# Performance work log

Hardware: AMD Instinct MI355X
Metric: run time of the kernel (lower is better)

The kernel has to match this reference:

```python
import jax, jax.numpy as jnp
import numpy as np

N_HEAD = 16


def setup_inputs() -> dict:
    key = jax.random.key(0)
    k1, k2, k3 = jax.random.split(key, 3)
    B, S, D = 2, 2048, 1024
    return {
        "hidden_states": jax.random.normal(k1, (B, S, D), dtype=jnp.float32),
        "c_attn_w": jax.random.normal(k2, (D, 3 * D), dtype=jnp.float32) * 0.02,
        "c_attn_b": jnp.zeros((3 * D,), dtype=jnp.float32),
        "c_proj_w": jax.random.normal(k3, (D, D), dtype=jnp.float32) * 0.02,
        "c_proj_b": jnp.zeros((D,), dtype=jnp.float32),
    }


def reference(hidden_states, c_attn_w, c_attn_b, c_proj_w, c_proj_b):
    B, S, D = hidden_states.shape
    H = N_HEAD
    hd = D // H
    # Fused QKV projection (Conv1D == linear with transposed weight layout)
    qkv = hidden_states @ c_attn_w + c_attn_b  # [B,S,3D]
    q, k, v = jnp.split(qkv, 3, axis=-1)
    # split heads -> [B,H,S,hd]
    q = q.reshape(B, S, H, hd).transpose(0, 2, 1, 3)
    k = k.reshape(B, S, H, hd).transpose(0, 2, 1, 3)
    v = v.reshape(B, S, H, hd).transpose(0, 2, 1, 3)
    # scaled dot-product with causal mask
    scores = jnp.einsum("bhqd,bhkd->bhqk", q, k) / jnp.asarray(hd ** 0.5, q.dtype)
    causal = jnp.tril(jnp.ones((S, S), dtype=bool))  # [S,S]
    mask_value = jnp.finfo(scores.dtype).min
    scores = jnp.where(causal[None, None, :, :], scores, mask_value)
    attn_weights = jax.nn.softmax(scores, axis=-1)  # [B,H,S,S]
    ctx = jnp.einsum("bhqk,bhkd->bhqd", attn_weights, v)  # [B,H,S,hd]
    ctx = ctx.transpose(0, 2, 1, 3).reshape(B, S, D)  # merge heads
    out = ctx @ c_proj_w + c_proj_b  # [B,S,D]
    return out
```

## Files before the change

### kernel.cpp

```cpp
#include <hip/hip_runtime.h>
#include <hip/hip_bf16.h>

typedef __attribute__((ext_vector_type(8))) short short8;
typedef __attribute__((ext_vector_type(4))) float f32x4;
typedef __attribute__((ext_vector_type(16))) float f32x16;
typedef __attribute__((ext_vector_type(4))) unsigned short u16x4;
typedef __attribute__((ext_vector_type(4))) unsigned int u32x4;

#define MFMA16(a, b, c) __builtin_amdgcn_mfma_f32_16x16x32_bf16((a), (b), (c), 0, 0, 0)
#define MFMA32(a, b, c) __builtin_amdgcn_mfma_f32_32x32x16_bf16((a), (b), (c), 0, 0, 0)

__device__ __forceinline__ unsigned short f2bf(float f) {
    union { float f; unsigned u; } v; v.f = f;
    return (unsigned short)((v.u + 0x7fffu + ((v.u >> 16) & 1u)) >> 16);
}

__device__ __forceinline__ unsigned cvtpk(float lo, float hi_) {
    unsigned r;
    asm volatile("v_cvt_pk_bf16_f32 %0, %1, %2" : "=v"(r) : "v"(lo), "v"(hi_));
    return r;
}

__global__ void cast_x_kernel(const float* __restrict__ x, ushort* __restrict__ y) {
    int i = blockIdx.x * blockDim.x + threadIdx.x;
    float4 v = ((const float4*)x)[i];
    u16x4 o = { f2bf(v.x), f2bf(v.y), f2bf(v.z), f2bf(v.w) };
    *(u16x4*)(y + (size_t)i * 4) = o;
}

__global__ void transpose_cast_kernel(const float* __restrict__ W, ushort* __restrict__ WT,
                                      int K, int N) {
    __shared__ ushort t[64][66];
    int n0 = blockIdx.x * 64, k0 = blockIdx.y * 64;
    int tn = threadIdx.x & 63, tg = threadIdx.x >> 6;
#pragma unroll
    for (int i = 0; i < 16; ++i) {
        int k = tg * 16 + i;
        t[tn][k] = f2bf(W[(size_t)(k0 + k) * N + n0 + tn]);
    }
    __syncthreads();
#pragma unroll
    for (int i = 0; i < 16; ++i) {
        int nn = tg * 16 + i;
        WT[(size_t)(n0 + nn) * K + k0 + tn] = t[nn][tn];
    }
}

#define QSCALE 0.18033688011112042f

template <int MODE>
__global__ __launch_bounds__(256)
void gemm_bt_kernel(const ushort* __restrict__ A, const ushort* __restrict__ BT,
                    const float* __restrict__ bias,
                    ushort* __restrict__ Qb, ushort* __restrict__ Kb,
                    ushort* __restrict__ VT, float* __restrict__ Out,
                    int M, int N, int K) {
    __shared__ ushort Asm[2][128 * 64];
    __shared__ ushort Bsm[2][128 * 64];
    const int lane = threadIdx.x & 63;
    const int wv = threadIdx.x >> 6;
    const int l15 = lane & 15, lg = lane >> 4;
    const int rm = (wv >> 1) * 64, cn = (wv & 1) * 64;
    const int row0 = blockIdx.y * 128, col0 = blockIdx.x * 128;

    const char* Agb = (const char*)(A + (size_t)row0 * K);
    const char* Bgb = (const char*)(BT + (size_t)col0 * K);
    const size_t rowbytes = (size_t)K * 2;

    f32x4 acc[4][4];
#pragma unroll
    for (int mi = 0; mi < 4; ++mi)
#pragma unroll
        for (int ni = 0; ni < 4; ++ni) acc[mi][ni] = f32x4{0.f, 0.f, 0.f, 0.f};

    const int grow_l = (lane >> 3);
    const int gcol_l = (lane & 7) * 16;

#define GSTAGE(buf, k0_)                                                                \
    do {                                                                                \
        _Pragma("unroll")                                                               \
        for (int c_ = 0; c_ < 4; ++c_) {                                                \
            int chunk = wv * 4 + c_;                              \
            size_t go = (size_t)(chunk * 8 + grow_l) * rowbytes + (size_t)(k0_)*2 +     \
                        gcol_l;                                                         \
            int lo = chunk * 1024 + lane * 16;                                          \
            __builtin_amdgcn_global_load_lds(                                           \
                (const __attribute__((address_space(1))) void*)(Agb + go),              \
                (__attribute__((address_space(3))) void*)((char*)&Asm[buf][0] + lo),    \
                16, 0, 0);                                                              \
            __builtin_amdgcn_global_load_lds(                                           \
                (const __attribute__((address_space(1))) void*)(Bgb + go),              \
                (__attribute__((address_space(3))) void*)((char*)&Bsm[buf][0] + lo),    \
                16, 0, 0);                                                              \
        }                                                                               \
    } while (0)

    GSTAGE(0, 0);
    __syncthreads();

    int cur = 0;
    for (int k0 = 0; k0 < K; k0 += 64) {
        if (k0 + 64 < K) GSTAGE(cur ^ 1, k0 + 64);
#pragma unroll
        for (int ks = 0; ks < 2; ++ks) {
            short8 af[4], bf[4];
#pragma unroll
            for (int mi = 0; mi < 4; ++mi)
                af[mi] = *(const short8*)&Asm[cur][(rm + mi * 16 + l15) * 64 + ks * 32 + lg * 8];
#pragma unroll
            for (int ni = 0; ni < 4; ++ni)
                bf[ni] = *(const short8*)&Bsm[cur][(cn + ni * 16 + l15) * 64 + ks * 32 + lg * 8];
#pragma unroll
            for (int mi = 0; mi < 4; ++mi)
#pragma unroll
                for (int ni = 0; ni < 4; ++ni)
                    acc[mi][ni] = MFMA16(af[mi], bf[ni], acc[mi][ni]);
        }
        __syncthreads();
        cur ^= 1;
    }
#undef GSTAGE

    if (MODE == 0) {
        const int sect = col0 >> 10;
#pragma unroll
        for (int ni = 0; ni < 4; ++ni) {
            int col = col0 + cn + ni * 16 + l15;
            float bv = bias[col];
            int dcol = col & 1023, h = dcol >> 6, dd = dcol & 63;
#pragma unroll
            for (int mi = 0; mi < 4; ++mi) {
                int mrow0 = row0 + rm + mi * 16 + lg * 4;
                if (sect == 2) {
                    int b = mrow0 >> 11, s = mrow0 & 2047;
                    u16x4 o;
#pragma unroll
                    for (int j = 0; j < 4; ++j) o[j] = f2bf(acc[mi][ni][j] + bv);
                    *(u16x4*)&VT[((size_t)((b << 4) + h) * 64 + dd) * 2048 + s] = o;
                } else {
                    ushort* dst = sect ? Kb : Qb;
                    float sc = sect ? 1.f : QSCALE;
#pragma unroll
                    for (int j = 0; j < 4; ++j) {
                        int tok = mrow0 + j;
                        int b = tok >> 11, s = tok & 2047;
                        dst[((size_t)((b << 4) + h) * 2048 + s) * 64 + dd] =
                            f2bf((acc[mi][ni][j] + bv) * sc);
                    }
                }
            }
        }
    } else {
#pragma unroll
        for (int ni = 0; ni < 4; ++ni) {
            int col = col0 + cn + ni * 16 + l15;
            float bv = bias[col];
#pragma unroll
            for (int mi = 0; mi < 4; ++mi) {
                int mrow0 = row0 + rm + mi * 16 + lg * 4;
#pragma unroll
                for (int j = 0; j < 4; ++j)
                    Out[(size_t)(mrow0 + j) * N + col] = acc[mi][ni][j] + bv;
            }
        }
    }
}

__global__ __launch_bounds__(256)
void attn_kernel(const ushort* __restrict__ Qb, const ushort* __restrict__ Kb,
                 const ushort* __restrict__ VT, ushort* __restrict__ CTX) {
    __shared__ __align__(16) ushort Ksm[2][64 * 64];
    __shared__ __align__(16) ushort Vsm[2][64 * 64];

    const int tid = threadIdx.x;
    const int lane = tid & 63;
    const int w = tid >> 6;
    const int l31 = lane & 31;
    const int hi = lane >> 5;
    const int r7 = l31 & 7;

    const int id = blockIdx.x;
    const int xcd = id & 7, jj = id >> 3;
    const int bh = (xcd << 2) + (jj >> 4);
    const int qt = ((jj >> 5) & 1) ? (jj & 15) : 15 - (jj & 15);
    const int qw0 = qt * 128 + w * 32;
    const int qrow = qw0 + l31;

    const ushort* Qh = Qb + (size_t)bh * 2048 * 64;
    const ushort* Kh = Kb + (size_t)bh * 2048 * 64;
    const ushort* Vh = VT + (size_t)bh * 64 * 2048;

    short8 qf[4];
#pragma unroll
    for (int dc = 0; dc < 4; ++dc)
        qf[dc] = *(const short8*)&Qh[(size_t)qrow * 64 + dc * 16 + hi * 8];

    const int srow = tid >> 3;
    const int scol = tid & 7;
    const int swz8 = (scol ^ (srow & 7)) * 8;

    u32x4 kr0, kr1, vr0, vr1;

#define LDREGS(kb_)                                                                     \
    do {                                                                                \
        const ushort* kp = Kh + (size_t)((kb_) + srow) * 64 + scol * 8;                 \
        kr0 = *(const u32x4*)kp;                                                        \
        kr1 = *(const u32x4*)(kp + 32 * 64);                                            \
        const ushort* vp = Vh + (size_t)srow * 2048 + (kb_) + scol * 8;                 \
        vr0 = *(const u32x4*)vp;                                                        \
        vr1 = *(const u32x4*)(vp + (size_t)32 * 2048);                                  \
    } while (0)

#define DSWRITE(buf)                                                                    \
    do {                                                                                \
        ushort* kd = &Ksm[buf][srow * 64 + swz8];                                       \
        *(u32x4*)kd = kr0;                                                              \
        *(u32x4*)(kd + 32 * 64) = kr1;                                                  \
        ushort* vd = &Vsm[buf][srow * 64 + swz8];                                       \
        *(u32x4*)vd = vr0;                                                              \
        *(u32x4*)(vd + 32 * 64) = vr1;                                                  \
    } while (0)

    const int nc = 2 * qt + 2;
    const int cdiag = 2 * qt + (w >> 1);

    LDREGS(0);
    DSWRITE(0);
    __syncthreads();

    float mrun = -1e30f, lsum = 0.f;
    f32x16 acc0, acc1;
#pragma unroll
    for (int r = 0; r < 16; ++r) { acc0[r] = 0.f; acc1[r] = 0.f; }

    int cur = 0;
    for (int c = 0; c < nc; ++c) {
        const int kb = c * 64;
        const bool havenext = (c + 1 < nc);
        if (havenext) LDREGS(kb + 64);

        if (!(w < 2 && c == nc - 1)) {
            const ushort* Kc = &Ksm[cur][0];
            const ushort* Vc = &Vsm[cur][0];

            short8 kf0[4], kf1[4];
#pragma unroll
            for (int dc = 0; dc < 4; ++dc) {
                kf0[dc] = *(const short8*)(Kc + l31 * 64 + (((dc * 2 + hi) ^ r7) << 3));
                kf1[dc] = *(const short8*)(Kc + (32 + l31) * 64 + (((dc * 2 + hi) ^ r7) << 3));
            }

            f32x16 st0, st1;
#pragma unroll
            for (int r = 0; r < 16; ++r) { st0[r] = 0.f; st1[r] = 0.f; }
            __builtin_amdgcn_s_setprio(1);
#pragma unroll
            for (int dc = 0; dc < 4; ++dc) {
                st0 = MFMA32(kf0[dc], qf[dc], st0);
                st1 = MFMA32(kf1[dc], qf[dc], st1);
            }
            __builtin_amdgcn_s_setprio(0);

            if (c == cdiag) {
                const int base0 = kb + (hi << 2);
                const int base1 = kb + 32 + (hi << 2);
#pragma unroll
                for (int r = 0; r < 16; ++r) {
                    int k0 = base0 + ((r & 3) + 8 * (r >> 2));
                    int k1 = base1 + ((r & 3) + 8 * (r >> 2));
                    st0[r] = (k0 <= qrow) ? st0[r] : -1e30f;
                    st1[r] = (k1 <= qrow) ? st1[r] : -1e30f;
                }
            }

            short8 vg0[4], vg1[4];
#pragma unroll
            for (int g = 0; g < 4; ++g) {
                vg0[g] = *(const short8*)(Vc + l31 * 64 + (((2 * g + hi) ^ r7) << 3));
                vg1[g] = *(const short8*)(Vc + (32 + l31) * 64 + (((2 * g + hi) ^ r7) << 3));
            }

            float tmax = st0[0];
#pragma unroll
            for (int r = 1; r < 16; ++r) tmax = fmaxf(tmax, st0[r]);
#pragma unroll
            for (int r = 0; r < 16; ++r) tmax = fmaxf(tmax, st1[r]);
            tmax = fmaxf(tmax, __shfl_xor(tmax, 32));

            if (!__all(tmax <= mrun + 8.0f)) {
                float mnew = fmaxf(mrun, tmax);
                float sc = exp2f(mrun - mnew);
#pragma unroll
                for (int r = 0; r < 16; ++r) { acc0[r] *= sc; acc1[r] *= sc; }
                lsum *= sc;
                mrun = mnew;
            }

            float tsum = 0.f;
#pragma unroll
            for (int r = 0; r < 16; ++r) { st0[r] = exp2f(st0[r] - mrun); tsum += st0[r]; }
#pragma unroll
            for (int r = 0; r < 16; ++r) { st1[r] = exp2f(st1[r] - mrun); tsum += st1[r]; }
            lsum += tsum;

            if (havenext) DSWRITE(cur ^ 1);

#define MAKE_PFRAG(st, kcL, out)                                                        \
    do {                                                                                \
        unsigned c00 = cvtpk(st[8 * kcL + 0], st[8 * kcL + 1]);                         \
        unsigned c01 = cvtpk(st[8 * kcL + 2], st[8 * kcL + 3]);                         \
        unsigned c10 = cvtpk(st[8 * kcL + 4], st[8 * kcL + 5]);                         \
        unsigned c11 = cvtpk(st[8 * kcL + 6], st[8 * kcL + 7]);                         \
        unsigned e0 = hi ? c00 : c10, e1 = hi ? c01 : c11;                              \
        unsigned pa0 = e0, pb0 = e0, pa1 = e1, pb1 = e1;                                \
        asm volatile("v_permlane32_swap_b32 %0, %1" : "+v"(pa0), "+v"(pb0));            \
        asm volatile("v_permlane32_swap_b32 %0, %1" : "+v"(pa1), "+v"(pb1));            \
        unsigned rec0 = hi ? pa0 : pb0;                                                 \
        unsigned rec1 = hi ? pa1 : pb1;                                                 \
        u32x4 fw;                                                                       \
        fw.x = hi ? rec0 : c00;                                                         \
        fw.y = hi ? rec1 : c01;                                                         \
        fw.z = hi ? c10 : rec0;                                                         \
        fw.w = hi ? c11 : rec1;                                                         \
        out = __builtin_bit_cast(short8, fw);                                           \
    } while (0)

            short8 pf;
            __builtin_amdgcn_s_setprio(1);
            MAKE_PFRAG(st0, 0, pf);
            acc0 = MFMA32(vg0[0], pf, acc0);
            acc1 = MFMA32(vg1[0], pf, acc1);
            MAKE_PFRAG(st0, 1, pf);
            acc0 = MFMA32(vg0[1], pf, acc0);
            acc1 = MFMA32(vg1[1], pf, acc1);
            MAKE_PFRAG(st1, 0, pf);
            acc0 = MFMA32(vg0[2], pf, acc0);
            acc1 = MFMA32(vg1[2], pf, acc1);
            MAKE_PFRAG(st1, 1, pf);
            acc0 = MFMA32(vg0[3], pf, acc0);
            acc1 = MFMA32(vg1[3], pf, acc1);
            __builtin_amdgcn_s_setprio(0);
#undef MAKE_PFRAG
        } else {
            if (havenext) DSWRITE(cur ^ 1);
        }

        __syncthreads();
        cur ^= 1;
    }
#undef LDREGS
#undef DSWRITE

    lsum += __shfl_xor(lsum, 32);
    const float inv = 1.f / lsum;
    const int b = bh >> 4, h = bh & 15;
    const size_t tokrow = ((size_t)b * 2048 + qw0 + l31) * 1024 + (size_t)h * 64;

#define WRITE_DT(accv, dt)                                                              \
    do {                                                                                \
        _Pragma("unroll")                                                               \
        for (int q2 = 0; q2 < 4; ++q2) {                                                \
            int d0 = dt * 32 + 8 * q2 + (hi << 2);                                      \
            u16x4 o;                                                                    \
            _Pragma("unroll")                                                           \
            for (int j = 0; j < 4; ++j) o[j] = f2bf(accv[4 * q2 + j] * inv);            \
            *(u16x4*)&CTX[tokrow + d0] = o;                                             \
        }                                                                               \
    } while (0)

    WRITE_DT(acc0, 0);
    WRITE_DT(acc1, 1);
#undef WRITE_DT
}

extern "C" void kernel_launch(void* const* d_in, const int* in_sizes, int n_in,
                              void* d_out, int out_size, void* d_ws, size_t ws_size,
                              hipStream_t stream) {
    const float* X     = (const float*)d_in[0];
    const float* Wqkv  = (const float*)d_in[1];
    const float* bqkv  = (const float*)d_in[2];
    const float* Wproj = (const float*)d_in[3];
    const float* bproj = (const float*)d_in[4];
    float* Out = (float*)d_out;

    ushort* Xb     = (ushort*)d_ws;
    ushort* WqkvT  = Xb + (size_t)4096 * 1024;
    ushort* WprojT = WqkvT + (size_t)3072 * 1024;
    ushort* Qb     = WprojT + (size_t)1024 * 1024;
    ushort* Kb     = Qb + (size_t)4096 * 1024;
    ushort* VT     = Kb + (size_t)4096 * 1024;
    ushort* CTX    = VT + (size_t)4096 * 1024;

    cast_x_kernel<<<4096, 256, 0, stream>>>(X, Xb);
    transpose_cast_kernel<<<dim3(48, 16), 256, 0, stream>>>(Wqkv, WqkvT, 1024, 3072);
    transpose_cast_kernel<<<dim3(16, 16), 256, 0, stream>>>(Wproj, WprojT, 1024, 1024);
    gemm_bt_kernel<0><<<dim3(24, 32), 256, 0, stream>>>(Xb, WqkvT, bqkv, Qb, Kb, VT, nullptr,
                                                        4096, 3072, 1024);
    attn_kernel<<<512, 256, 0, stream>>>(Qb, Kb, VT, CTX);
    gemm_bt_kernel<1><<<dim3(8, 32), 256, 0, stream>>>(CTX, WprojT, bproj, nullptr, nullptr,
                                                       nullptr, Out, 4096, 1024, 1024);
}
```

Baseline: 149.4 us.

## Shrink GEMM K-tile to 32 with XOR-swizzled LDS and occupancy hint

```diff
diff --git a/kernel.cpp b/kernel.cpp
--- a/kernel.cpp
+++ b/kernel.cpp
@@ -49,16 +49,17 @@
 #define QSCALE 0.18033688011112042f
 
 template <int MODE>
-__global__ __launch_bounds__(256)
+__global__ __launch_bounds__(256, 3)
 void gemm_bt_kernel(const ushort* __restrict__ A, const ushort* __restrict__ BT,
                     const float* __restrict__ bias,
                     ushort* __restrict__ Qb, ushort* __restrict__ Kb,
                     ushort* __restrict__ VT, float* __restrict__ Out,
                     int M, int N, int K) {
-    __shared__ ushort Asm[2][128 * 64];
-    __shared__ ushort Bsm[2][128 * 64];
-    const int lane = threadIdx.x & 63;
-    const int wv = threadIdx.x >> 6;
+    __shared__ ushort Asm[2][128 * 32];
+    __shared__ ushort Bsm[2][128 * 32];
+    const int tid = threadIdx.x;
+    const int lane = tid & 63;
+    const int wv = tid >> 6;
     const int l15 = lane & 15, lg = lane >> 4;
     const int rm = (wv >> 1) * 64, cn = (wv & 1) * 64;
     const int row0 = blockIdx.y * 128, col0 = blockIdx.x * 128;
@@ -73,49 +74,58 @@
 #pragma unroll
         for (int ni = 0; ni < 4; ++ni) acc[mi][ni] = f32x4{0.f, 0.f, 0.f, 0.f};
 
-    const int grow_l = (lane >> 3);
-    const int gcol_l = (lane & 7) * 16;
+    const int sr0 = tid >> 2, sc0 = (tid & 3) ^ (sr0 & 3);
+    const int sr1 = (tid + 256) >> 2, sc1 = (tid & 3) ^ (sr1 & 3);
 
 #define GSTAGE(buf, k0_)                                                                \
     do {                                                                                \
-        _Pragma("unroll")                                                               \
-        for (int c_ = 0; c_ < 4; ++c_) {                                                \
-            int chunk = wv * 4 + c_;                              \
-            size_t go = (size_t)(chunk * 8 + grow_l) * rowbytes + (size_t)(k0_)*2 +     \
-                        gcol_l;                                                         \
-            int lo = chunk * 1024 + lane * 16;                                          \
-            __builtin_amdgcn_global_load_lds(                                           \
-                (const __attribute__((address_space(1))) void*)(Agb + go),              \
-                (__attribute__((address_space(3))) void*)((char*)&Asm[buf][0] + lo),    \
-                16, 0, 0);                                                              \
-            __builtin_amdgcn_global_load_lds(                                           \
-                (const __attribute__((address_space(1))) void*)(Bgb + go),              \
-                (__attribute__((address_space(3))) void*)((char*)&Bsm[buf][0] + lo),    \
-                16, 0, 0);                                                              \
-        }                                                                               \
+        size_t kbyte = (size_t)(k0_)*2;                                                 \
+        __builtin_amdgcn_global_load_lds(                                               \
+            (const __attribute__((address_space(1))) void*)(Agb + (size_t)sr0 *         \
+                rowbytes + kbyte + sc0 * 16),                                           \
+            (__attribute__((address_space(3))) void*)((char*)&Asm[buf][0] + tid * 16),  \
+            16, 0, 0);                                                                  \
+        __builtin_amdgcn_global_load_lds(                                               \
+            (const __attribute__((address_space(1))) void*)(Agb + (size_t)sr1 *         \
+                rowbytes + kbyte + sc1 * 16),                                           \
+            (__attribute__((address_space(3))) void*)((char*)&Asm[buf][0] + 4096 +      \
+                tid * 16),                                                              \
+            16, 0, 0);                                                                  \
+        __builtin_amdgcn_global_load_lds(                                               \
+            (const __attribute__((address_space(1))) void*)(Bgb + (size_t)sr0 *         \
+                rowbytes + kbyte + sc0 * 16),                                           \
+            (__attribute__((address_space(3))) void*)((char*)&Bsm[buf][0] + tid * 16),  \
+            16, 0, 0);                                                                  \
+        __builtin_amdgcn_global_load_lds(                                               \
+            (const __attribute__((address_space(1))) void*)(Bgb + (size_t)sr1 *         \
+                rowbytes + kbyte + sc1 * 16),                                           \
+            (__attribute__((address_space(3))) void*)((char*)&Bsm[buf][0] + 4096 +      \
+                tid * 16),                                                              \
+            16, 0, 0);                                                                  \
     } while (0)
 
     GSTAGE(0, 0);
     __syncthreads();
 
+    const int sw8 = (lg ^ (l15 & 3)) << 3;
+
     int cur = 0;
-    for (int k0 = 0; k0 < K; k0 += 64) {
-        if (k0 + 64 < K) GSTAGE(cur ^ 1, k0 + 64);
-#pragma unroll
-        for (int ks = 0; ks < 2; ++ks) {
-            short8 af[4], bf[4];
-#pragma unroll
-            for (int mi = 0; mi < 4; ++mi)
-                af[mi] = *(const short8*)&Asm[cur][(rm + mi * 16 + l15) * 64 + ks * 32 + lg * 8];
+    for (int k0 = 0; k0 < K; k0 += 32) {
+        if (k0 + 32 < K) GSTAGE(cur ^ 1, k0 + 32);
+        short8 af[4], bf[4];
+#pragma unroll
+        for (int mi = 0; mi < 4; ++mi)
+            af[mi] = *(const short8*)&Asm[cur][(rm + mi * 16 + l15) * 32 + sw8];
+#pragma unroll
+        for (int ni = 0; ni < 4; ++ni)
+            bf[ni] = *(const short8*)&Bsm[cur][(cn + ni * 16 + l15) * 32 + sw8];
+        __builtin_amdgcn_s_setprio(1);
+#pragma unroll
+        for (int mi = 0; mi < 4; ++mi)
 #pragma unroll
             for (int ni = 0; ni < 4; ++ni)
-                bf[ni] = *(const short8*)&Bsm[cur][(cn + ni * 16 + l15) * 64 + ks * 32 + lg * 8];
-#pragma unroll
-            for (int mi = 0; mi < 4; ++mi)
-#pragma unroll
-                for (int ni = 0; ni < 4; ++ni)
-                    acc[mi][ni] = MFMA16(af[mi], bf[ni], acc[mi][ni]);
-        }
+                acc[mi][ni] = MFMA16(af[mi], bf[ni], acc[mi][ni]);
+        __builtin_amdgcn_s_setprio(0);
         __syncthreads();
         cur ^= 1;
     }
```

After: 130.3 us. 12.8% less time.
